# Kernel tuning notes

Hardware: AMD Instinct MI355X
Metric: run time of the kernel (lower is better)

Reference implementation:

```python
import jax, jax.numpy as jnp
import numpy as np
import math

WINDOW = 512
N_HEAD = 16

def setup_inputs() -> dict:
    key = jax.random.key(0)
    ks = jax.random.split(key, 5)
    B, L, D = 2, 4096, 1024
    s = 0.02
    return {
        "x": jax.random.normal(ks[0], (B, L, D), dtype=jnp.float32),
        "Wq": jax.random.normal(ks[1], (D, D), dtype=jnp.float32) * s,
        "bq": jnp.zeros((D,), jnp.float32),
        "Wk": jax.random.normal(ks[2], (D, D), dtype=jnp.float32) * s,
        "bk": jnp.zeros((D,), jnp.float32),
        "Wv": jax.random.normal(ks[3], (D, D), dtype=jnp.float32) * s,
        "bv": jnp.zeros((D,), jnp.float32),
        "Wo": jax.random.normal(ks[4], (D, D), dtype=jnp.float32) * s,
        "bo": jnp.zeros((D,), jnp.float32),
    }

def reference(x, Wq, bq, Wk, bk, Wv, bv, Wo, bo):
    # Chunked sliding-window MHA (eval mode, dropout inactive).
    B, L, D = x.shape
    W, H = WINDOW, N_HEAD
    dh = D // H
    C = L // W  # number of query chunks
    scale = 1.0 / math.sqrt(dh)

    # Project full sequence once (linear, per-token -> identical math).
    q = x @ Wq.T + bq
    k = x @ Wk.T + bk
    v = x @ Wv.T + bv

    # Pad K/V by one window at the front so every chunk sees 2W keys.
    kp = jnp.pad(k, ((0, 0), (W, 0), (0, 0)))
    vp = jnp.pad(v, ((0, 0), (W, 0), (0, 0)))
    idx = jnp.arange(C)[:, None] * W + jnp.arange(2 * W)[None, :]  # [C, 2W] into padded seq
    kc = kp[:, idx].reshape(B, C, 2 * W, H, dh)
    vc = vp[:, idx].reshape(B, C, 2 * W, H, dh)
    qc = q.reshape(B, C, W, H, dh)

    scores = jnp.einsum('bcqhd,bckhd->bchqk', qc, kc) * scale  # [B,C,H,W,2W]
    valid = (idx >= W)  # padded positions (chunk 0's lookback) are invalid
    scores = jnp.where(valid[None, :, None, None, :], scores, jnp.float32(-1e9))
    attn = jax.nn.softmax(scores, axis=-1)
    out = jnp.einsum('bchqk,bckhd->bcqhd', attn, vc).reshape(B, L, D)
    return out @ Wo.T + bo
```

## Files before the change

### kernel.cpp

```cpp
#include <hip/hip_runtime.h>
#include <hip/hip_bf16.h>

typedef __hip_bfloat16 bf16;
typedef __attribute__((ext_vector_type(8))) short bf16x8;
typedef __attribute__((ext_vector_type(4))) float f32x4;
typedef unsigned int u32;
typedef unsigned short u16;

#define MFMA(a,b,c) __builtin_amdgcn_mfma_f32_16x16x32_bf16((a),(b),(c),0,0,0)

__device__ __forceinline__ u16 f32_to_bf16_rtne(float f) {
  u32 b = __builtin_bit_cast(u32, f);
  b += 0x7FFFu + ((b >> 16) & 1u);
  return (u16)(b >> 16);
}
__device__ __forceinline__ float bf16_to_f32(u16 h) {
  return __builtin_bit_cast(float, (u32)h << 16);
}
__device__ __forceinline__ u32 pk2bf(float a, float b) {
  u32 ua = __builtin_bit_cast(u32, a); ua += 0x7FFFu + ((ua >> 16) & 1u);
  u32 ub = __builtin_bit_cast(u32, b); ub += 0x7FFFu + ((ub >> 16) & 1u);
  return __builtin_amdgcn_perm(ub, ua, 0x07060302u);
}

__device__ __forceinline__ void barrier_lgkm() {
  asm volatile("s_waitcnt lgkmcnt(0)\n\ts_barrier" ::: "memory");
}

static constexpr float SL2E = 0.125f * 1.44269504f;

__global__ void detect_mode(const u16* __restrict__ x_raw, int* __restrict__ flag) {
  __shared__ int cnt;
  if (threadIdx.x == 0) cnt = 0;
  __syncthreads();
  int ok = 0;
  for (int i = threadIdx.x; i < 1024; i += 256) {
    const int e = (x_raw[2 * i] >> 7) & 0xFF;
    if (e >= 117 && e <= 137) ok++;
  }
  atomicAdd(&cnt, ok);
  __syncthreads();
  if (threadIdx.x == 0) *flag = (cnt < 512) ? 1 : 0;
}

__device__ __forceinline__ void cast8(const void* src, u16* dst, int mode, size_t i) {
  union { u16 h[8]; uint4 v; } u;
  if (mode) {
    const float4* s = (const float4*)src + i * 2;
    const float4 a = s[0], b = s[1];
    u.h[0] = f32_to_bf16_rtne(a.x); u.h[1] = f32_to_bf16_rtne(a.y);
    u.h[2] = f32_to_bf16_rtne(a.z); u.h[3] = f32_to_bf16_rtne(a.w);
    u.h[4] = f32_to_bf16_rtne(b.x); u.h[5] = f32_to_bf16_rtne(b.y);
    u.h[6] = f32_to_bf16_rtne(b.z); u.h[7] = f32_to_bf16_rtne(b.w);
  } else {
    u.v = ((const uint4*)src)[i];
  }
  ((uint4*)dst)[i] = u.v;
}

__global__ __launch_bounds__(256)
void cast_all(const void* __restrict__ x,
              const void* __restrict__ wq, const void* __restrict__ wk,
              const void* __restrict__ wv, const void* __restrict__ wo,
              u16* __restrict__ xb, u16* __restrict__ wqkv,
              u16* __restrict__ wob, const int* __restrict__ flag) {
  const int mode = *flag;
  const int bid = blockIdx.x;
  if (bid < 4096) {
    cast8(x, xb, mode, (size_t)bid * 256 + threadIdx.x);
  } else {
    const size_t DD8 = (size_t)1024 * 1024 / 8;
    const int m = (bid - 4096) >> 9;
    const size_t i = ((size_t)((bid - 4096) & 511)) * 256 + threadIdx.x;
    const void* src = (m == 0) ? wq : (m == 1) ? wk : (m == 2) ? wv : wo;
    u16* dst = (m < 3) ? (wqkv + (size_t)m * DD8 * 8) : wob;
    cast8(src, dst, mode, i);
  }
}

template <int MODE>
__global__ __launch_bounds__(256)
void gemm_bt(const bf16* __restrict__ A, const bf16* __restrict__ W,
             const void* __restrict__ b0, const void* __restrict__ b1,
             const void* __restrict__ b2, void* __restrict__ o0,
             void* __restrict__ o1, void* __restrict__ o2,
             const int* __restrict__ flag, int M, int N, int K)
{
  __shared__ bf16 As[128 * 64];
  __shared__ bf16 Bs[128 * 64];

  const int mode = *flag;
  const int tid  = threadIdx.x;
  const int wave = tid >> 6, lane = tid & 63;
  const int quad = lane >> 4, l16 = lane & 15;
  const int wm   = wave >> 1, wn  = wave & 1;
  const int m0   = blockIdx.x * 128, n0 = blockIdx.y * 128;

  const int band = n0 >> 10;
  const void* bias = (band == 0) ? b0 : (band == 1) ? b1 : b2;

  const int srow = lane >> 3;
  const int sg   = lane & 7;
  const size_t rgs = (size_t)8 * K;
  const bf16* aSrc = A + (size_t)(m0 + wave * 32 + srow) * K + sg * 8;
  const bf16* wSrc = W + (size_t)(n0 + wave * 32 + srow) * K + sg * 8;
  bf16* aDst = As + (wave * 32 + srow) * 64 + ((sg ^ srow) * 8);
  bf16* wDst = Bs + (wave * 32 + srow) * 64 + ((sg ^ srow) * 8);

  const int niter = K >> 6;

  uint4 a0 = *(const uint4*)(aSrc);
  uint4 a1 = *(const uint4*)(aSrc + rgs);
  uint4 a2 = *(const uint4*)(aSrc + 2 * rgs);
  uint4 a3 = *(const uint4*)(aSrc + 3 * rgs);
  uint4 w0 = *(const uint4*)(wSrc);
  uint4 w1 = *(const uint4*)(wSrc + rgs);
  uint4 w2 = *(const uint4*)(wSrc + 2 * rgs);
  uint4 w3 = *(const uint4*)(wSrc + 3 * rgs);
  aSrc += 64; wSrc += 64;

  f32x4 acc[4][4] = {};

  const int arow[4] = { (wm * 64 + 0 * 16 + l16) * 64, (wm * 64 + 1 * 16 + l16) * 64,
                        (wm * 64 + 2 * 16 + l16) * 64, (wm * 64 + 3 * 16 + l16) * 64 };
  const int brow[4] = { (wn * 64 + 0 * 16 + l16) * 64, (wn * 64 + 1 * 16 + l16) * 64,
                        (wn * 64 + 2 * 16 + l16) * 64, (wn * 64 + 3 * 16 + l16) * 64 };
  const int r7 = l16 & 7;

  for (int t = 0; t < niter; ++t) {
    if (t) barrier_lgkm();
    *(uint4*)(aDst)        = a0;
    *(uint4*)(aDst + 512)  = a1;
    *(uint4*)(aDst + 1024) = a2;
    *(uint4*)(aDst + 1536) = a3;
    *(uint4*)(wDst)        = w0;
    *(uint4*)(wDst + 512)  = w1;
    *(uint4*)(wDst + 1024) = w2;
    *(uint4*)(wDst + 1536) = w3;
    barrier_lgkm();
    if (t + 1 < niter) {
      a0 = *(const uint4*)(aSrc);
      a1 = *(const uint4*)(aSrc + rgs);
      a2 = *(const uint4*)(aSrc + 2 * rgs);
      a3 = *(const uint4*)(aSrc + 3 * rgs);
      w0 = *(const uint4*)(wSrc);
      w1 = *(const uint4*)(wSrc + rgs);
      w2 = *(const uint4*)(wSrc + 2 * rgs);
      w3 = *(const uint4*)(wSrc + 3 * rgs);
      aSrc += 64; wSrc += 64;
    }
#pragma unroll
    for (int kk = 0; kk < 2; ++kk) {
      bf16x8 af[4], bw[4];
#pragma unroll
      for (int mt = 0; mt < 4; ++mt)
        af[mt] = *(const bf16x8*)(As + arow[mt] + (((kk * 4 + quad) ^ r7) * 8));
#pragma unroll
      for (int nt = 0; nt < 4; ++nt)
        bw[nt] = *(const bf16x8*)(Bs + brow[nt] + (((kk * 4 + quad) ^ r7) * 8));
#pragma unroll
      for (int mt = 0; mt < 4; ++mt)
#pragma unroll
        for (int nt = 0; nt < 4; ++nt)
          acc[mt][nt] = MFMA(af[mt], bw[nt], acc[mt][nt]);
    }
  }

#pragma unroll
  for (int nt = 0; nt < 4; ++nt) {
    const int col = n0 + wn * 64 + nt * 16 + l16;
    const int cl  = col & 1023;
    const float bv = mode ? ((const float*)bias)[cl]
                          : bf16_to_f32(((const u16*)bias)[cl]);
#pragma unroll
    for (int mt = 0; mt < 4; ++mt) {
      const int rbase = m0 + wm * 64 + mt * 16 + quad * 4;
      if (MODE == 1) {
#pragma unroll
        for (int r = 0; r < 4; ++r) {
          const float val = acc[mt][nt][r] + bv;
          const size_t idx = (size_t)(rbase + r) * N + col;
          if (mode) ((float*)o0)[idx] = val;
          else      ((u16*)o0)[idx]   = f32_to_bf16_rtne(val);
        }
      } else if (band == 2) {
        const int hh = cl >> 6, dd = cl & 63;
        const int bb = rbase >> 12, tl = rbase & 4095;
        u16* dst = (u16*)o2 + ((size_t)((bb * 16 + hh) * 64 + dd)) * 4096 + tl;
        uint2 pk;
        pk.x = pk2bf(acc[mt][nt][0] + bv, acc[mt][nt][1] + bv);
        pk.y = pk2bf(acc[mt][nt][2] + bv, acc[mt][nt][3] + bv);
        *(uint2*)dst = pk;
      } else {
        u16* dst = (u16*)((band == 0) ? o0 : o1);
        const float sc = (band == 0) ? SL2E : 1.0f;
#pragma unroll
        for (int r = 0; r < 4; ++r)
          dst[(size_t)(rbase + r) * 1024 + cl] =
              f32_to_bf16_rtne((acc[mt][nt][r] + bv) * sc);
      }
    }
  }
}

__global__ __launch_bounds__(256)
void attn_swin(const bf16* __restrict__ qb, const bf16* __restrict__ kb,
               const bf16* __restrict__ vtb, u16* __restrict__ ctx)
{
  __shared__ __align__(16) bf16 Ks[64 * 72];
  __shared__ __align__(16) bf16 Vts[64 * 72];

  int bid = blockIdx.x;
  const int g  = bid & 255, qt = bid >> 8;
  const int h  = g & 15, c = (g >> 4) & 7, b = g >> 7;

  const int tid  = threadIdx.x;
  const int w    = tid >> 6, lane = tid & 63;
  const int quad = lane >> 4, l16 = lane & 15;

  const int tq0  = c * 512 + qt * 128;
  const int hoff = h * 64;
  const int kstart = (c == 0) ? 0 : (c - 1) * 512;
  const int nkt    = (c == 0) ? 8 : 16;

  bf16x8 qf[2][2];
#pragma unroll
  for (int u = 0; u < 2; ++u) {
    const bf16* qr = qb + ((size_t)(b * 4096 + tq0 + w * 32 + u * 16 + l16)) * 1024 + hoff;
    qf[u][0] = *(const bf16x8*)(qr + quad * 8);
    qf[u][1] = *(const bf16x8*)(qr + 32 + quad * 8);
  }

  const int m    = tid >> 2;
  const int cseg = (tid & 3) * 16;
  const int sig  = (((m >> 4) & 1) << 5) | (((m >> 2) & 3) << 3)
                 | (((m >> 5) & 1) << 2) | (m & 3);
  const bf16* kgp = kb + ((size_t)(b * 4096 + kstart + sig)) * 1024 + hoff + cseg;
  const bf16* vgp = vtb + ((size_t)((b * 16 + h) * 64 + m)) * 4096 + kstart + cseg;
  bf16* kdst = Ks  + m * 72 + cseg;
  bf16* vdst = Vts + m * 72 + cseg;

  float l_i[2] = {0.f, 0.f};
  f32x4 o[2][4] = {};

  uint4 ka0 = *(const uint4*)(kgp), ka1 = *(const uint4*)(kgp + 8);
  uint4 va0 = *(const uint4*)(vgp), va1 = *(const uint4*)(vgp + 8);
  kgp += (size_t)64 * 1024; vgp += 64;

  for (int t = 0; t < nkt; ++t) {
    uint4 kb0, kb1, vb0, vb1;
    if (t + 1 < nkt) {
      kb0 = *(const uint4*)(kgp); kb1 = *(const uint4*)(kgp + 8);
      vb0 = *(const uint4*)(vgp); vb1 = *(const uint4*)(vgp + 8);
      kgp += (size_t)64 * 1024; vgp += 64;
    }
    *(uint4*)(kdst) = ka0; *(uint4*)(kdst + 8) = ka1;
    *(uint4*)(vdst) = va0; *(uint4*)(vdst + 8) = va1;
    barrier_lgkm();

    f32x4 s[2][4] = {};
#pragma unroll
    for (int kt = 0; kt < 4; ++kt) {
      const bf16* kr = Ks + (kt * 16 + l16) * 72;
      bf16x8 kf0 = *(const bf16x8*)(kr + quad * 8);
      bf16x8 kf1 = *(const bf16x8*)(kr + 32 + quad * 8);
      s[0][kt] = MFMA(kf0, qf[0][0], s[0][kt]);
      s[0][kt] = MFMA(kf1, qf[0][1], s[0][kt]);
      s[1][kt] = MFMA(kf0, qf[1][0], s[1][kt]);
      s[1][kt] = MFMA(kf1, qf[1][1], s[1][kt]);
    }

    typedef union { u32 d[4]; bf16x8 v; } fragu;
    fragu pf[2][2];
#pragma unroll
    for (int u = 0; u < 2; ++u) {
      float rs = 0.f;
#pragma unroll
      for (int kt = 0; kt < 4; ++kt)
#pragma unroll
        for (int r = 0; r < 4; ++r) {
          const float p = __builtin_amdgcn_exp2f(s[u][kt][r]);
          s[u][kt][r] = p;
          rs += p;
        }
      rs += __shfl_xor(rs, 16);
      rs += __shfl_xor(rs, 32);
      l_i[u] += rs;
#pragma unroll
      for (int hh = 0; hh < 2; ++hh)
#pragma unroll
        for (int dw = 0; dw < 4; ++dw) {
          const int kt = 2 * (dw >> 1) + hh, r0 = 2 * (dw & 1);
          pf[u][hh].d[dw] = pk2bf(s[u][kt][r0], s[u][kt][r0 + 1]);
        }
    }

#pragma unroll
    for (int dt = 0; dt < 4; ++dt) {
      const bf16* vr = Vts + (dt * 16 + l16) * 72;
      bf16x8 vf0 = *(const bf16x8*)(vr + quad * 8);
      bf16x8 vf1 = *(const bf16x8*)(vr + 32 + quad * 8);
      o[0][dt] = MFMA(vf0, pf[0][0].v, o[0][dt]);
      o[0][dt] = MFMA(vf1, pf[0][1].v, o[0][dt]);
      o[1][dt] = MFMA(vf0, pf[1][0].v, o[1][dt]);
      o[1][dt] = MFMA(vf1, pf[1][1].v, o[1][dt]);
    }
    barrier_lgkm();

    ka0 = kb0; ka1 = kb1; va0 = vb0; va1 = vb1;
  }

#pragma unroll
  for (int u = 0; u < 2; ++u) {
    const float inv = 1.0f / l_i[u];
    const int qrow = tq0 + w * 32 + u * 16 + l16;
    u16* crow = ctx + ((size_t)(b * 4096 + qrow)) * 1024 + hoff;
#pragma unroll
    for (int dt = 0; dt < 4; ++dt) {
      uint2 pk;
      pk.x = pk2bf(o[u][dt][0] * inv, o[u][dt][1] * inv);
      pk.y = pk2bf(o[u][dt][2] * inv, o[u][dt][3] * inv);
      *(uint2*)(crow + dt * 16 + quad * 4) = pk;
    }
  }
}

extern "C" void kernel_launch(void* const* d_in, const int* in_sizes, int n_in,
                              void* d_out, int out_size, void* d_ws, size_t ws_size,
                              hipStream_t stream) {
  const void* x  = d_in[0];
  const void* Wq = d_in[1];
  const void* bq = d_in[2];
  const void* Wk = d_in[3];
  const void* bk = d_in[4];
  const void* Wv = d_in[5];
  const void* bv = d_in[6];
  const void* Wo = d_in[7];
  const void* bo = d_in[8];

  const size_t MD = (size_t)8192 * 1024;
  const size_t DD = (size_t)1024 * 1024;

  char* ws = (char*)d_ws;
  int*  flag  = (int*)ws;                     ws += 256;
  u16*  xb    = (u16*)ws;                     ws += MD * 2;
  u16*  Wqkvb = (u16*)ws;                     ws += 3 * DD * 2;
  u16*  Wob   = (u16*)ws;                     ws += DD * 2;
  u16*  qbuf  = (u16*)ws;                     ws += MD * 2;
  u16*  kbuf  = (u16*)ws;                     ws += MD * 2;
  u16*  vtb   = (u16*)ws;                     ws += MD * 2;
  u16*  ctx   = (u16*)ws;

  detect_mode<<<dim3(1), dim3(256), 0, stream>>>((const u16*)x, flag);
  cast_all<<<dim3(6144), dim3(256), 0, stream>>>(x, Wq, Wk, Wv, Wo,
                                                 xb, Wqkvb, Wob, flag);

  gemm_bt<0><<<dim3(64, 24), dim3(256), 0, stream>>>(
      (const bf16*)xb, (const bf16*)Wqkvb, bq, bk, bv,
      qbuf, kbuf, vtb, flag, 8192, 3072, 1024);

  attn_swin<<<dim3(1024), dim3(256), 0, stream>>>(
      (const bf16*)qbuf, (const bf16*)kbuf, (const bf16*)vtb, ctx);

  gemm_bt<1><<<dim3(64, 8), dim3(256), 0, stream>>>(
      (const bf16*)ctx, (const bf16*)Wob, bo, bo, bo,
      d_out, nullptr, nullptr, flag, 8192, 1024, 1024);
}
```

Before: 254.0 us.

## Double-buffer K/V tiles in LDS and use truncating bf16 pack for P

The attention loop now keeps two LDS buffers for K and V^T. The next tile is written into one buffer while the current tile is computed from the other, which halves the barriers per tile. This is meant to overlap the LDS stores and global loads with the MFMA work. The probability pack also changes from round-to-nearest-even to truncation, saving ALU ops but adding a small bias to P.

```diff
diff --git a/kernel.cpp b/kernel.cpp
--- a/kernel.cpp
+++ b/kernel.cpp
@@ -21,6 +21,10 @@
   u32 ua = __builtin_bit_cast(u32, a); ua += 0x7FFFu + ((ua >> 16) & 1u);
   u32 ub = __builtin_bit_cast(u32, b); ub += 0x7FFFu + ((ub >> 16) & 1u);
   return __builtin_amdgcn_perm(ub, ua, 0x07060302u);
+}
+__device__ __forceinline__ u32 pk2bf_rtz(float a, float b) {
+  return __builtin_amdgcn_perm(__builtin_bit_cast(u32, b),
+                               __builtin_bit_cast(u32, a), 0x07060302u);
 }
 
 __device__ __forceinline__ void barrier_lgkm() {
@@ -207,8 +211,8 @@
 void attn_swin(const bf16* __restrict__ qb, const bf16* __restrict__ kb,
                const bf16* __restrict__ vtb, u16* __restrict__ ctx)
 {
-  __shared__ __align__(16) bf16 Ks[64 * 72];
-  __shared__ __align__(16) bf16 Vts[64 * 72];
+  __shared__ __align__(16) bf16 Ks[2][64 * 72];
+  __shared__ __align__(16) bf16 Vts[2][64 * 72];
 
   int bid = blockIdx.x;
   const int g  = bid & 255, qt = bid >> 8;
@@ -237,8 +241,7 @@
                  | (((m >> 5) & 1) << 2) | (m & 3);
   const bf16* kgp = kb + ((size_t)(b * 4096 + kstart + sig)) * 1024 + hoff + cseg;
   const bf16* vgp = vtb + ((size_t)((b * 16 + h) * 64 + m)) * 4096 + kstart + cseg;
-  bf16* kdst = Ks  + m * 72 + cseg;
-  bf16* vdst = Vts + m * 72 + cseg;
+  const int soff = m * 72 + cseg;
 
   float l_i[2] = {0.f, 0.f};
   f32x4 o[2][4] = {};
@@ -246,22 +249,20 @@
   uint4 ka0 = *(const uint4*)(kgp), ka1 = *(const uint4*)(kgp + 8);
   uint4 va0 = *(const uint4*)(vgp), va1 = *(const uint4*)(vgp + 8);
   kgp += (size_t)64 * 1024; vgp += 64;
-
-  for (int t = 0; t < nkt; ++t) {
-    uint4 kb0, kb1, vb0, vb1;
-    if (t + 1 < nkt) {
-      kb0 = *(const uint4*)(kgp); kb1 = *(const uint4*)(kgp + 8);
-      vb0 = *(const uint4*)(vgp); vb1 = *(const uint4*)(vgp + 8);
-      kgp += (size_t)64 * 1024; vgp += 64;
-    }
-    *(uint4*)(kdst) = ka0; *(uint4*)(kdst + 8) = ka1;
-    *(uint4*)(vdst) = va0; *(uint4*)(vdst + 8) = va1;
-    barrier_lgkm();
-
+  *(uint4*)(Ks[0] + soff) = ka0; *(uint4*)(Ks[0] + soff + 8) = ka1;
+  *(uint4*)(Vts[0] + soff) = va0; *(uint4*)(Vts[0] + soff + 8) = va1;
+  ka0 = *(const uint4*)(kgp); ka1 = *(const uint4*)(kgp + 8);
+  va0 = *(const uint4*)(vgp); va1 = *(const uint4*)(vgp + 8);
+  kgp += (size_t)64 * 1024; vgp += 64;
+  barrier_lgkm();
+
+  typedef union { u32 d[4]; bf16x8 v; } fragu;
+
+  auto compute = [&](const bf16* ksb, const bf16* vtsb) {
     f32x4 s[2][4] = {};
 #pragma unroll
     for (int kt = 0; kt < 4; ++kt) {
-      const bf16* kr = Ks + (kt * 16 + l16) * 72;
+      const bf16* kr = ksb + (kt * 16 + l16) * 72;
       bf16x8 kf0 = *(const bf16x8*)(kr + quad * 8);
       bf16x8 kf1 = *(const bf16x8*)(kr + 32 + quad * 8);
       s[0][kt] = MFMA(kf0, qf[0][0], s[0][kt]);
@@ -269,8 +270,6 @@
       s[1][kt] = MFMA(kf0, qf[1][0], s[1][kt]);
       s[1][kt] = MFMA(kf1, qf[1][1], s[1][kt]);
     }
-
-    typedef union { u32 d[4]; bf16x8 v; } fragu;
     fragu pf[2][2];
 #pragma unroll
     for (int u = 0; u < 2; ++u) {
@@ -291,13 +290,12 @@
 #pragma unroll
         for (int dw = 0; dw < 4; ++dw) {
           const int kt = 2 * (dw >> 1) + hh, r0 = 2 * (dw & 1);
-          pf[u][hh].d[dw] = pk2bf(s[u][kt][r0], s[u][kt][r0 + 1]);
+          pf[u][hh].d[dw] = pk2bf_rtz(s[u][kt][r0], s[u][kt][r0 + 1]);
         }
     }
-
 #pragma unroll
     for (int dt = 0; dt < 4; ++dt) {
-      const bf16* vr = Vts + (dt * 16 + l16) * 72;
+      const bf16* vr = vtsb + (dt * 16 + l16) * 72;
       bf16x8 vf0 = *(const bf16x8*)(vr + quad * 8);
       bf16x8 vf1 = *(const bf16x8*)(vr + 32 + quad * 8);
       o[0][dt] = MFMA(vf0, pf[0][0].v, o[0][dt]);
@@ -305,9 +303,30 @@
       o[1][dt] = MFMA(vf0, pf[1][0].v, o[1][dt]);
       o[1][dt] = MFMA(vf1, pf[1][1].v, o[1][dt]);
     }
+  };
+
+  for (int t = 0; t < nkt; t += 2) {
+    *(uint4*)(Ks[1] + soff) = ka0; *(uint4*)(Ks[1] + soff + 8) = ka1;
+    *(uint4*)(Vts[1] + soff) = va0; *(uint4*)(Vts[1] + soff + 8) = va1;
+    if (t + 2 < nkt) {
+      ka0 = *(const uint4*)(kgp); ka1 = *(const uint4*)(kgp + 8);
+      va0 = *(const uint4*)(vgp); va1 = *(const uint4*)(vgp + 8);
+      kgp += (size_t)64 * 1024; vgp += 64;
+    }
+    compute(Ks[0], Vts[0]);
     barrier_lgkm();
 
-    ka0 = kb0; ka1 = kb1; va0 = vb0; va1 = vb1;
+    if (t + 2 < nkt) {
+      *(uint4*)(Ks[0] + soff) = ka0; *(uint4*)(Ks[0] + soff + 8) = ka1;
+      *(uint4*)(Vts[0] + soff) = va0; *(uint4*)(Vts[0] + soff + 8) = va1;
+      if (t + 3 < nkt) {
+        ka0 = *(const uint4*)(kgp); ka1 = *(const uint4*)(kgp + 8);
+        va0 = *(const uint4*)(vgp); va1 = *(const uint4*)(vgp + 8);
+        kgp += (size_t)64 * 1024; vgp += 64;
+      }
+    }
+    compute(Ks[1], Vts[1]);
+    barrier_lgkm();
   }
 
 #pragma unroll
```

Result: faster. 238.6 us (-6.1%).
